# Optimization experiments

Measured on AMD Instinct MI355X. Metric: run time of the kernel, lower is better.

## Reference

```python
import jax, jax.numpy as jnp
import numpy as np

N_HEAD = 16
HEAD_DIM = 64
N_EMBD = N_HEAD * HEAD_DIM
KS, STRIDE = 4, 4
LN_EPS = 1e-5


def _layernorm(x, g, b):
    mu = jnp.mean(x, axis=-1, keepdims=True)
    var = jnp.var(x, axis=-1, keepdims=True)
    return (x - mu) * jax.lax.rsqrt(var + LN_EPS) * g + b


def _depthwise_conv(x_bcl, w):
    # x_bcl: [N, head_dim, L], w: [head_dim, 1, KS] (torch Conv1d groups=head_dim layout)
    return jax.lax.conv_general_dilated(
        x_bcl, w, window_strides=(STRIDE,), padding='VALID',
        dimension_numbers=('NCH', 'OIH', 'NCH'), feature_group_count=HEAD_DIM)


def setup_inputs() -> dict:
    key = jax.random.key(0)
    ks = jax.random.split(key, 12)
    B, T, L = 8, 64, 4096
    s = 0.02
    return {
        'x': jax.random.normal(ks[0], (B, T, N_EMBD), jnp.float32),
        'cached_k': jax.random.normal(ks[1], (B, N_HEAD, L, HEAD_DIM), jnp.float32),
        'cached_v': jax.random.normal(ks[2], (B, N_HEAD, L, HEAD_DIM), jnp.float32),
        'w_attn': jax.random.normal(ks[3], (N_EMBD, 3 * N_EMBD), jnp.float32) * s,
        'b_attn': jnp.zeros((3 * N_EMBD,), jnp.float32),
        'w_proj': jax.random.normal(ks[4], (N_EMBD, N_EMBD), jnp.float32) * s,
        'b_proj': jnp.zeros((N_EMBD,), jnp.float32),
        'k_conv': jax.random.normal(ks[5], (HEAD_DIM, 1, KS), jnp.float32) * 0.5,
        'v_conv': jax.random.normal(ks[6], (HEAD_DIM, 1, KS), jnp.float32) * 0.5,
        'ln_k_g': jnp.ones((HEAD_DIM,), jnp.float32),
        'ln_k_b': jnp.zeros((HEAD_DIM,), jnp.float32),
        'ln_v_g': jnp.ones((HEAD_DIM,), jnp.float32),
        'ln_v_b': jnp.zeros((HEAD_DIM,), jnp.float32),
    }


def reference(x, cached_k, cached_v, w_attn, b_attn, w_proj, b_proj,
              k_conv, v_conv, ln_k_g, ln_k_b, ln_v_g, ln_v_b):
    B, T, C = x.shape
    H, hd = N_HEAD, HEAD_DIM
    qkv = x @ w_attn + b_attn                      # [B,T,3C]
    q, k, v = jnp.split(qkv, 3, axis=-1)
    q = q.reshape(B, T, H, hd).transpose(0, 2, 1, 3)  # [B,H,T,hd]
    k = k.reshape(B, T, H, hd).transpose(0, 2, 1, 3)
    v = v.reshape(B, T, H, hd).transpose(0, 2, 1, 3)

    # compress cached K/V: depthwise conv over cache length, then LayerNorm
    L = cached_k.shape[2]
    pk = cached_k.transpose(0, 1, 3, 2).reshape(B * H, hd, L)
    pv = cached_v.transpose(0, 1, 3, 2).reshape(B * H, hd, L)
    ck = _depthwise_conv(pk, k_conv).reshape(B, H, hd, -1).transpose(0, 1, 3, 2)  # [B,H,Lc,hd]
    cv = _depthwise_conv(pv, v_conv).reshape(B, H, hd, -1).transpose(0, 1, 3, 2)
    ck = jax.lax.stop_gradient(_layernorm(ck, ln_k_g, ln_k_b))
    cv = jax.lax.stop_gradient(_layernorm(cv, ln_v_g, ln_v_b))

    k_full = jnp.concatenate([ck, k], axis=2)      # [B,H,Tk,hd]
    v_full = jnp.concatenate([cv, v], axis=2)
    Tk = k_full.shape[2]

    # faithful to original: rectangular tril(T, Tk) -> query i sees keys j<=i
    mask = jnp.tril(jnp.ones((T, Tk), dtype=bool))
    att = jnp.einsum('bhqd,bhkd->bhqk', q, k_full) * (1.0 / np.sqrt(hd))
    att = jnp.where(mask[None, None], att, -jnp.inf)
    att = jax.nn.softmax(att, axis=-1)
    y = jnp.einsum('bhqk,bhkd->bhqd', att, v_full)
    y = y.transpose(0, 2, 1, 3).reshape(B, T, C)
    return y @ w_proj + b_proj
```

## Files before the change

kernel.cpp:

```cpp
#include <hip/hip_runtime.h>
#include <math.h>

#define NH 16
#define LCACHE 4096

typedef __attribute__((ext_vector_type(8))) short short8;
typedef __attribute__((ext_vector_type(8))) unsigned short ushort8;
typedef __attribute__((ext_vector_type(4))) float f32x4;

__device__ __forceinline__ unsigned short f2bf(float f) {
    unsigned int u = __float_as_uint(f);
    u = (u + 0x7fffu + ((u >> 16) & 1u)) >> 16;
    return (unsigned short)u;
}

__global__ __launch_bounds__(256)
void pack_kernel(const float* __restrict__ x, const float* __restrict__ w_attn,
                 const float* __restrict__ w_proj,
                 ushort* __restrict__ xp, ushort* __restrict__ wq,
                 ushort* __restrict__ wp)
{
    __shared__ float Wt[64][65];
    const int bid = blockIdx.x, tid = threadIdx.x;
    const int w = tid >> 6, l = tid & 63;

    if (bid < 512) {
        const int isP = (bid >= 256);
        const int g2  = bid & 255;
        const int ntw = g2 >> 4, ktw = g2 & 15;
        const float* W = isP ? w_proj : w_attn;
        const int ldw  = isP ? 1024 : 3072;
        ushort* D      = isP ? wp : wq;
#pragma unroll
        for (int rep = 0; rep < 16; ++rep) {
            int lin = rep * 256 + tid;
            int kr = lin >> 6, nn = lin & 63;
            Wt[kr][nn] = W[(size_t)(ktw * 64 + kr) * ldw + ntw * 64 + nn];
        }
        __syncthreads();
        int r = l & 15, kg8 = l >> 4;
#pragma unroll
        for (int e = 0; e < 2; ++e) {
            int bi = w + e * 4;
            int kb = bi >> 2, nb = bi & 3;
            ushort8 o;
#pragma unroll
            for (int j = 0; j < 8; ++j)
                o[j] = f2bf(Wt[kb * 32 + kg8 * 8 + j][nb * 16 + r]);
            size_t f_lin = (size_t)(ntw * 16 + ktw) * 8 + bi;
            *(ushort8*)(D + f_lin * 512 + l * 8) = o;
        }
        return;
    }

    {
        int bid2 = bid - 512;
        int r = l & 15, kg8 = l >> 4;
#pragma unroll
        for (int i = 0; i < 4; ++i) {
            int f = bid2 * 16 + w * 4 + i;
            int mt = f >> 6, kt = (f >> 2) & 15, fi = f & 3;
            int kb = fi >> 1, mb = fi & 1;
            int m  = mt * 32 + mb * 16 + r;
            int k0 = kt * 64 + kb * 32 + kg8 * 8;
            const float* s = x + (size_t)m * 1024 + k0;
            ushort8 o;
#pragma unroll
            for (int j = 0; j < 8; ++j) o[j] = f2bf(s[j]);
            *(ushort8*)(xp + (size_t)f * 512 + l * 8) = o;
        }
    }
}

__global__ __launch_bounds__(512, 2)
void attn_kernel(const float* __restrict__ cached_k, const float* __restrict__ cached_v,
                 const float* __restrict__ kcw, const float* __restrict__ vcw,
                 const float* __restrict__ lkg, const float* __restrict__ lkb,
                 const float* __restrict__ lvg, const float* __restrict__ lvb,
                 const float* __restrict__ b_attn,
                 const ushort* __restrict__ xp, const ushort* __restrict__ wq,
                 ushort* __restrict__ yp)
{
    __shared__ __align__(16) float qs[32][68];
    __shared__ __align__(16) ushort P_lds[2048];
    __shared__ __align__(16) ushort ckf_s[4096];
    __shared__ __align__(16) ushort cvf_s[4096];

    const int bid = blockIdx.x;
    const int h    = ((bid & 7) << 1) | ((bid >> 3) & 1);
    const int rem  = bid >> 4;
    const int b    = rem >> 1;
    const int half = rem & 1;
    const int mtA  = b * 2 + half;

    const int tid = threadIdx.x;
    const int w = tid >> 6, l = tid & 63;
    const int c = l & 15, rg = l >> 4;
    const int g = w & 1, dup = w >> 1;

    {
        ushort8 z = {0,0,0,0,0,0,0,0};
        ((ushort8*)ckf_s)[tid] = z;
        ((ushort8*)cvf_s)[tid] = z;
    }
    __syncthreads();

    if (w >= 4) {
        const int cw = w - 4;
        const int NR = half ? 64 : 32;
        const float* Kb = cached_k + (size_t)(b * NH + h) * (LCACHE * 64);
        const float* Vb = cached_v + (size_t)(b * NH + h) * (LCACHE * 64);
        float4 wk = *(const float4*)(kcw + l * 4);
        float4 wv = *(const float4*)(vcw + l * 4);
        float gk = lkg[l], bk = lkb[l], gv = lvg[l], bv = lvb[l];

        const int iters = (2 * NR) / 4;
        for (int it = 0; it < iters; it += 4) {
            float tap[4][4]; int isKv[4], lcv[4];
#pragma unroll
            for (int q = 0; q < 4; ++q) {
                int t = cw + (it + q) * 4;
                isKv[q] = (t < NR);
                int lc = isKv[q] ? t : t - NR;
                lcv[q] = lc;
                const float* p = (isKv[q] ? Kb : Vb) + (size_t)lc * 256 + l;
                tap[q][0] = p[0]; tap[q][1] = p[64]; tap[q][2] = p[128]; tap[q][3] = p[192];
            }
            float av[4], s1[4], s2[4];
#pragma unroll
            for (int q = 0; q < 4; ++q) {
                float4 cwv = isKv[q] ? wk : wv;
                float a = tap[q][0] * cwv.x;
                a = fmaf(tap[q][1], cwv.y, a);
                a = fmaf(tap[q][2], cwv.z, a);
                a = fmaf(tap[q][3], cwv.w, a);
                av[q] = a; s1[q] = a; s2[q] = a * a;
            }
#pragma unroll
            for (int o = 32; o; o >>= 1) {
#pragma unroll
                for (int q = 0; q < 4; ++q) {
                    s1[q] += __shfl_xor(s1[q], o);
                    s2[q] += __shfl_xor(s2[q], o);
                }
            }
#pragma unroll
            for (int q = 0; q < 4; ++q) {
                float mu  = s1[q] * 0.015625f;
                float var = s2[q] * 0.015625f - mu * mu;
                float gg = isKv[q] ? gk : gv, bb2 = isKv[q] ? bk : bv;
                float outv = (av[q] - mu) * rsqrtf(var + 1e-5f) * gg + bb2;
                unsigned short bf = f2bf(outv);
                int key = lcv[q], d = l;
                if (isKv[q]) {
                    int off = ((key >> 4) * 2 + (d >> 5)) * 512
                            + ((d >> 3) & 3) * 128 + (key & 15) * 8 + (d & 7);
                    ckf_s[off] = bf;
                } else {
                    int off = ((d >> 4) * 2 + (key >> 5)) * 512
                            + ((key >> 3) & 3) * 128 + (d & 15) * 8 + (key & 7);
                    cvf_s[off] = bf;
                }
            }
        }
    } else {
        const ushort* ab = xp + (size_t)mtA * 32768;
        const ushort* bb = wq + (size_t)h * 65536;
        f32x4 acc0 = {0.f,0.f,0.f,0.f}, acc1 = {0.f,0.f,0.f,0.f};
#pragma unroll
        for (int kt = 0; kt < 16; ++kt) {
            const ushort* A = ab + kt * 2048;
            const ushort* B = bb + kt * 4096;
            short8 a00 = *(const short8*)(A + l * 8);
            short8 a01 = *(const short8*)(A + 512 + l * 8);
            short8 a10 = *(const short8*)(A + 1024 + l * 8);
            short8 a11 = *(const short8*)(A + 1536 + l * 8);
            short8 b0  = *(const short8*)(B + (size_t)w * 512 + l * 8);
            short8 b1  = *(const short8*)(B + (size_t)(4 + w) * 512 + l * 8);
            acc0 = __builtin_amdgcn_mfma_f32_16x16x32_bf16(a00, b0, acc0, 0, 0, 0);
            acc1 = __builtin_amdgcn_mfma_f32_16x16x32_bf16(a01, b0, acc1, 0, 0, 0);
            acc0 = __builtin_amdgcn_mfma_f32_16x16x32_bf16(a10, b1, acc0, 0, 0, 0);
            acc1 = __builtin_amdgcn_mfma_f32_16x16x32_bf16(a11, b1, acc1, 0, 0, 0);
        }
        const int n = w * 16 + c;
        float bv2 = b_attn[h * 64 + n];
#pragma unroll
        for (int mb = 0; mb < 2; ++mb) {
            f32x4 acc = mb ? acc1 : acc0;
#pragma unroll
            for (int rr = 0; rr < 4; ++rr)
                qs[mb * 16 + rg * 4 + rr][n] = (acc[rr] + bv2) * 0.125f;
        }
    }
    __syncthreads();

    short8 akf[4][2];
#pragma unroll
    for (int mf = 0; mf < 4; ++mf)
#pragma unroll
        for (int kf = 0; kf < 2; ++kf)
            akf[mf][kf] = *(const short8*)&ckf_s[(mf * 2 + kf) * 512 + l * 8];
    short8 avf[2];
#pragma unroll
    for (int kf = 0; kf < 2; ++kf)
        avf[kf] = *(const short8*)&cvf_s[(dup * 2 + kf) * 512 + l * 8];

    short8 qb[2];
#pragma unroll
    for (int kf = 0; kf < 2; ++kf) {
        int row = 16 * g + c;
        int d0  = 32 * kf + 8 * rg;
        float4 v0 = *(const float4*)&qs[row][d0];
        float4 v1 = *(const float4*)&qs[row][d0 + 4];
        ushort8 t;
        t[0] = f2bf(v0.x); t[1] = f2bf(v0.y); t[2] = f2bf(v0.z); t[3] = f2bf(v0.w);
        t[4] = f2bf(v1.x); t[5] = f2bf(v1.y); t[6] = f2bf(v1.z); t[7] = f2bf(v1.w);
        qb[kf] = (short8)t;
    }

    f32x4 sacc[4];
#pragma unroll
    for (int mf = 0; mf < 4; ++mf) { sacc[mf][0]=0.f; sacc[mf][1]=0.f; sacc[mf][2]=0.f; sacc[mf][3]=0.f; }
#pragma unroll
    for (int mf = 0; mf < 4; ++mf) {
        sacc[mf] = __builtin_amdgcn_mfma_f32_16x16x32_bf16(akf[mf][0], qb[0], sacc[mf], 0, 0, 0);
        sacc[mf] = __builtin_amdgcn_mfma_f32_16x16x32_bf16(akf[mf][1], qb[1], sacc[mf], 0, 0, 0);
    }

    const int gq = half * 32 + 16 * g + c;
    float pv[4][4];
    float mx = -3.0e38f;
#pragma unroll
    for (int mf = 0; mf < 4; ++mf)
#pragma unroll
        for (int rr = 0; rr < 4; ++rr) {
            int kidx = 16 * mf + 4 * rg + rr;
            float sc = (kidx <= gq) ? sacc[mf][rr] : -3.0e38f;
            pv[mf][rr] = sc;
            mx = fmaxf(mx, sc);
        }
    mx = fmaxf(mx, __shfl_xor(mx, 16));
    mx = fmaxf(mx, __shfl_xor(mx, 32));
    float sum = 0.f;
#pragma unroll
    for (int mf = 0; mf < 4; ++mf)
#pragma unroll
        for (int rr = 0; rr < 4; ++rr) {
            int kidx = 16 * mf + 4 * rg + rr;
            float e = (kidx <= gq) ? __expf(pv[mf][rr] - mx) : 0.f;
            pv[mf][rr] = e;
            sum += e;
        }
    sum += __shfl_xor(sum, 16);
    sum += __shfl_xor(sum, 32);
    float inv = 1.0f / sum;

    if (dup == 0) {
        int q = 16 * g + c;
        int swz = (q & 7) << 3;
#pragma unroll
        for (int mf = 0; mf < 4; ++mf)
#pragma unroll
            for (int rr = 0; rr < 4; ++rr) {
                int kidx = 16 * mf + 4 * rg + rr;
                P_lds[q * 64 + (kidx ^ swz)] = f2bf(pv[mf][rr] * inv);
            }
    }
    __syncthreads();

    short8 pb[2];
#pragma unroll
    for (int kf = 0; kf < 2; ++kf) {
        int q = 16 * g + c;
        int key0 = 32 * kf + 8 * rg;
        pb[kf] = *(const short8*)&P_lds[q * 64 + (key0 ^ ((q & 7) << 3))];
    }
    f32x4 oacc = {0.f, 0.f, 0.f, 0.f};
    oacc = __builtin_amdgcn_mfma_f32_16x16x32_bf16(avf[0], pb[0], oacc, 0, 0, 0);
    oacc = __builtin_amdgcn_mfma_f32_16x16x32_bf16(avf[1], pb[1], oacc, 0, 0, 0);

#pragma unroll
    for (int rr = 0; rr < 4; ++rr) {
        int d  = 16 * dup + 4 * rg + rr;
        int kb = d >> 5, ke = d & 31;
        int l2 = ((ke >> 3) << 4) | c;
        int j2 = ke & 7;
        size_t off = (size_t)mtA * 32768 + (size_t)h * 2048
                   + (size_t)(kb * 2 + g) * 512 + (size_t)l2 * 8 + j2;
        yp[off] = f2bf(oacc[rr]);
    }
}

__global__ __launch_bounds__(512, 2)
void gemm2_kernel(const ushort* __restrict__ Ap, const ushort* __restrict__ Bp,
                  const float* __restrict__ bias, float* __restrict__ C)
{
    __shared__ float red[32][68];

    const int bid = blockIdx.x;
    const int nt = ((bid & 7) << 1) | ((bid >> 3) & 1);
    const int mt = bid >> 4;
    const int tid = threadIdx.x;
    const int w = tid >> 6, l = tid & 63;
    const int kg = w >> 2, w4 = w & 3;
    const int c = l & 15, rg = l >> 4;

    const ushort* ab = Ap + (size_t)mt * 32768;
    const ushort* bb = Bp + (size_t)nt * 65536;
    f32x4 acc0 = {0.f,0.f,0.f,0.f}, acc1 = {0.f,0.f,0.f,0.f};
#pragma unroll
    for (int s = 0; s < 8; ++s) {
        const int kt = kg * 8 + s;
        const ushort* A = ab + kt * 2048;
        const ushort* B = bb + kt * 4096;
        short8 a00 = *(const short8*)(A + l * 8);
        short8 a01 = *(const short8*)(A + 512 + l * 8);
        short8 a10 = *(const short8*)(A + 1024 + l * 8);
        short8 a11 = *(const short8*)(A + 1536 + l * 8);
        short8 b0  = *(const short8*)(B + (size_t)w4 * 512 + l * 8);
        short8 b1  = *(const short8*)(B + (size_t)(4 + w4) * 512 + l * 8);
        acc0 = __builtin_amdgcn_mfma_f32_16x16x32_bf16(a00, b0, acc0, 0, 0, 0);
        acc1 = __builtin_amdgcn_mfma_f32_16x16x32_bf16(a01, b0, acc1, 0, 0, 0);
        acc0 = __builtin_amdgcn_mfma_f32_16x16x32_bf16(a10, b1, acc0, 0, 0, 0);
        acc1 = __builtin_amdgcn_mfma_f32_16x16x32_bf16(a11, b1, acc1, 0, 0, 0);
    }

    const int nl = w4 * 16 + c;
    if (kg == 0) {
#pragma unroll
        for (int mb = 0; mb < 2; ++mb) {
            f32x4 acc = mb ? acc1 : acc0;
#pragma unroll
            for (int rr = 0; rr < 4; ++rr)
                red[mb * 16 + rg * 4 + rr][nl] = acc[rr];
        }
    }
    __syncthreads();
    if (kg == 1) {
        float bv = bias[nt * 64 + nl];
#pragma unroll
        for (int mb = 0; mb < 2; ++mb) {
            f32x4 acc = mb ? acc1 : acc0;
#pragma unroll
            for (int rr = 0; rr < 4; ++rr) {
                int m = mb * 16 + rg * 4 + rr;
                C[(size_t)(mt * 32 + m) * 1024 + nt * 64 + nl] =
                    red[m][nl] + acc[rr] + bv;
            }
        }
    }
}

extern "C" void kernel_launch(void* const* d_in, const int* in_sizes, int n_in,
                              void* d_out, int out_size, void* d_ws, size_t ws_size,
                              hipStream_t stream)
{
    const float* x        = (const float*)d_in[0];
    const float* cached_k = (const float*)d_in[1];
    const float* cached_v = (const float*)d_in[2];
    const float* w_attn   = (const float*)d_in[3];
    const float* b_attn   = (const float*)d_in[4];
    const float* w_proj   = (const float*)d_in[5];
    const float* b_proj   = (const float*)d_in[6];
    const float* k_conv   = (const float*)d_in[7];
    const float* v_conv   = (const float*)d_in[8];
    const float* ln_k_g   = (const float*)d_in[9];
    const float* ln_k_b   = (const float*)d_in[10];
    const float* ln_v_g   = (const float*)d_in[11];
    const float* ln_v_b   = (const float*)d_in[12];

    ushort* xp = (ushort*)d_ws;
    ushort* wq = xp + 524288;
    ushort* wp = wq + 1048576;
    ushort* yp = wp + 1048576;
    float* out = (float*)d_out;

    pack_kernel<<<576, 256, 0, stream>>>(x, w_attn, w_proj, xp, wq, wp);
    attn_kernel<<<256, 512, 0, stream>>>(cached_k, cached_v, k_conv, v_conv,
                                         ln_k_g, ln_k_b, ln_v_g, ln_v_b,
                                         b_attn, xp, wq, yp);
    gemm2_kernel<<<256, 512, 0, stream>>>(yp, wp, b_proj, out);
}
```

Measured before the change: 30.09 us.

## Interleave cache conv/LN with Q GEMM across all waves; split proj GEMM finer

The attention kernel no longer splits waves into separate compress and GEMM roles. Every wave now issues its cached K/V tap loads up front, runs half of a split-K Q projection, does the conv+LayerNorm, then loads the second V batch and runs the other half, reducing the two K halves through LDS. This is meant to hide global load latency behind MFMA work and use all eight waves for both jobs. The projection GEMM moves to 512 blocks with a 4-way K split, XCD-aware tile mapping and a smaller reduction buffer, and f2bf switches to the library bf16 conversion. The risks are higher register pressure from the 64 held tap values (the occupancy hint of 2 was removed) and extra LDS synchronisation.

```diff
diff --git a/kernel.cpp b/kernel.cpp
--- a/kernel.cpp
+++ b/kernel.cpp
@@ -1,4 +1,5 @@
 #include <hip/hip_runtime.h>
+#include <hip/hip_bf16.h>
 #include <math.h>
 
 #define NH 16
@@ -9,9 +10,10 @@
 typedef __attribute__((ext_vector_type(4))) float f32x4;
 
 __device__ __forceinline__ unsigned short f2bf(float f) {
-    unsigned int u = __float_as_uint(f);
-    u = (u + 0x7fffu + ((u >> 16) & 1u)) >> 16;
-    return (unsigned short)u;
+    __hip_bfloat16 b = __float2bfloat16(f);
+    unsigned short u;
+    __builtin_memcpy(&u, &b, 2);
+    return u;
 }
 
 __global__ __launch_bounds__(256)
@@ -72,7 +74,7 @@
     }
 }
 
-__global__ __launch_bounds__(512, 2)
+__global__ __launch_bounds__(512)
 void attn_kernel(const float* __restrict__ cached_k, const float* __restrict__ cached_v,
                  const float* __restrict__ kcw, const float* __restrict__ vcw,
                  const float* __restrict__ lkg, const float* __restrict__ lkb,
@@ -83,8 +85,8 @@
 {
     __shared__ __align__(16) float qs[32][68];
     __shared__ __align__(16) ushort P_lds[2048];
-    __shared__ __align__(16) ushort ckf_s[4096];
-    __shared__ __align__(16) ushort cvf_s[4096];
+    __shared__ __align__(16) ushort ck_s[4096];
+    __shared__ __align__(16) ushort cv_s[4096];
 
     const int bid = blockIdx.x;
     const int h    = ((bid & 7) << 1) | ((bid >> 3) & 1);
@@ -95,221 +97,38 @@
 
     const int tid = threadIdx.x;
     const int w = tid >> 6, l = tid & 63;
+    const int kg = w >> 2, w4 = w & 3;
     const int c = l & 15, rg = l >> 4;
     const int g = w & 1, dup = w >> 1;
 
-    {
+    if (!half) {
         ushort8 z = {0,0,0,0,0,0,0,0};
-        ((ushort8*)ckf_s)[tid] = z;
-        ((ushort8*)cvf_s)[tid] = z;
+        ((ushort8*)cv_s)[tid] = z;
     }
     __syncthreads();
 
-    if (w >= 4) {
-        const int cw = w - 4;
-        const int NR = half ? 64 : 32;
-        const float* Kb = cached_k + (size_t)(b * NH + h) * (LCACHE * 64);
-        const float* Vb = cached_v + (size_t)(b * NH + h) * (LCACHE * 64);
-        float4 wk = *(const float4*)(kcw + l * 4);
-        float4 wv = *(const float4*)(vcw + l * 4);
-        float gk = lkg[l], bk = lkb[l], gv = lvg[l], bv = lvb[l];
-
-        const int iters = (2 * NR) / 4;
-        for (int it = 0; it < iters; it += 4) {
-            float tap[4][4]; int isKv[4], lcv[4];
-#pragma unroll
-            for (int q = 0; q < 4; ++q) {
-                int t = cw + (it + q) * 4;
-                isKv[q] = (t < NR);
-                int lc = isKv[q] ? t : t - NR;
-                lcv[q] = lc;
-                const float* p = (isKv[q] ? Kb : Vb) + (size_t)lc * 256 + l;
-                tap[q][0] = p[0]; tap[q][1] = p[64]; tap[q][2] = p[128]; tap[q][3] = p[192];
-            }
-            float av[4], s1[4], s2[4];
-#pragma unroll
-            for (int q = 0; q < 4; ++q) {
-                float4 cwv = isKv[q] ? wk : wv;
-                float a = tap[q][0] * cwv.x;
-                a = fmaf(tap[q][1], cwv.y, a);
-                a = fmaf(tap[q][2], cwv.z, a);
-                a = fmaf(tap[q][3], cwv.w, a);
-                av[q] = a; s1[q] = a; s2[q] = a * a;
-            }
-#pragma unroll
-            for (int o = 32; o; o >>= 1) {
-#pragma unroll
-                for (int q = 0; q < 4; ++q) {
-                    s1[q] += __shfl_xor(s1[q], o);
-                    s2[q] += __shfl_xor(s2[q], o);
-                }
-            }
-#pragma unroll
-            for (int q = 0; q < 4; ++q) {
-                float mu  = s1[q] * 0.015625f;
-                float var = s2[q] * 0.015625f - mu * mu;
-                float gg = isKv[q] ? gk : gv, bb2 = isKv[q] ? bk : bv;
-                float outv = (av[q] - mu) * rsqrtf(var + 1e-5f) * gg + bb2;
-                unsigned short bf = f2bf(outv);
-                int key = lcv[q], d = l;
-                if (isKv[q]) {
-                    int off = ((key >> 4) * 2 + (d >> 5)) * 512
-                            + ((d >> 3) & 3) * 128 + (key & 15) * 8 + (d & 7);
-                    ckf_s[off] = bf;
-                } else {
-                    int off = ((d >> 4) * 2 + (key >> 5)) * 512
-                            + ((key >> 3) & 3) * 128 + (d & 15) * 8 + (key & 7);
-                    cvf_s[off] = bf;
-                }
-            }
-        }
-    } else {
-        const ushort* ab = xp + (size_t)mtA * 32768;
-        const ushort* bb = wq + (size_t)h * 65536;
-        f32x4 acc0 = {0.f,0.f,0.f,0.f}, acc1 = {0.f,0.f,0.f,0.f};
-#pragma unroll
-        for (int kt = 0; kt < 16; ++kt) {
-            const ushort* A = ab + kt * 2048;
-            const ushort* B = bb + kt * 4096;
-            short8 a00 = *(const short8*)(A + l * 8);
-            short8 a01 = *(const short8*)(A + 512 + l * 8);
-            short8 a10 = *(const short8*)(A + 1024 + l * 8);
-            short8 a11 = *(const short8*)(A + 1536 + l * 8);
-            short8 b0  = *(const short8*)(B + (size_t)w * 512 + l * 8);
-            short8 b1  = *(const short8*)(B + (size_t)(4 + w) * 512 + l * 8);
-            acc0 = __builtin_amdgcn_mfma_f32_16x16x32_bf16(a00, b0, acc0, 0, 0, 0);
-            acc1 = __builtin_amdgcn_mfma_f32_16x16x32_bf16(a01, b0, acc1, 0, 0, 0);
-            acc0 = __builtin_amdgcn_mfma_f32_16x16x32_bf16(a10, b1, acc0, 0, 0, 0);
-            acc1 = __builtin_amdgcn_mfma_f32_16x16x32_bf16(a11, b1, acc1, 0, 0, 0);
-        }
-        const int n = w * 16 + c;
-        float bv2 = b_attn[h * 64 + n];
-#pragma unroll
-        for (int mb = 0; mb < 2; ++mb) {
-            f32x4 acc = mb ? acc1 : acc0;
-#pragma unroll
-            for (int rr = 0; rr < 4; ++rr)
-                qs[mb * 16 + rg * 4 + rr][n] = (acc[rr] + bv2) * 0.125f;
-        }
-    }
-    __syncthreads();
-
-    short8 akf[4][2];
-#pragma unroll
-    for (int mf = 0; mf < 4; ++mf)
-#pragma unroll
-        for (int kf = 0; kf < 2; ++kf)
-            akf[mf][kf] = *(const short8*)&ckf_s[(mf * 2 + kf) * 512 + l * 8];
-    short8 avf[2];
-#pragma unroll
-    for (int kf = 0; kf < 2; ++kf)
-        avf[kf] = *(const short8*)&cvf_s[(dup * 2 + kf) * 512 + l * 8];
-
-    short8 qb[2];
-#pragma unroll
-    for (int kf = 0; kf < 2; ++kf) {
-        int row = 16 * g + c;
-        int d0  = 32 * kf + 8 * rg;
-        float4 v0 = *(const float4*)&qs[row][d0];
-        float4 v1 = *(const float4*)&qs[row][d0 + 4];
-        ushort8 t;
-        t[0] = f2bf(v0.x); t[1] = f2bf(v0.y); t[2] = f2bf(v0.z); t[3] = f2bf(v0.w);
-        t[4] = f2bf(v1.x); t[5] = f2bf(v1.y); t[6] = f2bf(v1.z); t[7] = f2bf(v1.w);
-        qb[kf] = (short8)t;
-    }
-
-    f32x4 sacc[4];
-#pragma unroll
-    for (int mf = 0; mf < 4; ++mf) { sacc[mf][0]=0.f; sacc[mf][1]=0.f; sacc[mf][2]=0.f; sacc[mf][3]=0.f; }
-#pragma unroll
-    for (int mf = 0; mf < 4; ++mf) {
-        sacc[mf] = __builtin_amdgcn_mfma_f32_16x16x32_bf16(akf[mf][0], qb[0], sacc[mf], 0, 0, 0);
-        sacc[mf] = __builtin_amdgcn_mfma_f32_16x16x32_bf16(akf[mf][1], qb[1], sacc[mf], 0, 0, 0);
-    }
-
-    const int gq = half * 32 + 16 * g + c;
-    float pv[4][4];
-    float mx = -3.0e38f;
-#pragma unroll
-    for (int mf = 0; mf < 4; ++mf)
-#pragma unroll
-        for (int rr = 0; rr < 4; ++rr) {
-            int kidx = 16 * mf + 4 * rg + rr;
-            float sc = (kidx <= gq) ? sacc[mf][rr] : -3.0e38f;
-            pv[mf][rr] = sc;
-            mx = fmaxf(mx, sc);
-        }
-    mx = fmaxf(mx, __shfl_xor(mx, 16));
-    mx = fmaxf(mx, __shfl_xor(mx, 32));
-    float sum = 0.f;
-#pragma unroll
-    for (int mf = 0; mf < 4; ++mf)
-#pragma unroll
-        for (int rr = 0; rr < 4; ++rr) {
-            int kidx = 16 * mf + 4 * rg + rr;
-            float e = (kidx <= gq) ? __expf(pv[mf][rr] - mx) : 0.f;
-            pv[mf][rr] = e;
-            sum += e;
-        }
-    sum += __shfl_xor(sum, 16);
-    sum += __shfl_xor(sum, 32);
-    float inv = 1.0f / sum;
-
-    if (dup == 0) {
-        int q = 16 * g + c;
-        int swz = (q & 7) << 3;
-#pragma unroll
-        for (int mf = 0; mf < 4; ++mf)
-#pragma unroll
-            for (int rr = 0; rr < 4; ++rr) {
-                int kidx = 16 * mf + 4 * rg + rr;
-                P_lds[q * 64 + (kidx ^ swz)] = f2bf(pv[mf][rr] * inv);
-            }
-    }
-    __syncthreads();
-
-    short8 pb[2];
-#pragma unroll
-    for (int kf = 0; kf < 2; ++kf) {
-        int q = 16 * g + c;
-        int key0 = 32 * kf + 8 * rg;
-        pb[kf] = *(const short8*)&P_lds[q * 64 + (key0 ^ ((q & 7) << 3))];
-    }
-    f32x4 oacc = {0.f, 0.f, 0.f, 0.f};
-    oacc = __builtin_amdgcn_mfma_f32_16x16x32_bf16(avf[0], pb[0], oacc, 0, 0, 0);
-    oacc = __builtin_amdgcn_mfma_f32_16x16x32_bf16(avf[1], pb[1], oacc, 0, 0, 0);
-
-#pragma unroll
-    for (int rr = 0; rr < 4; ++rr) {
-        int d  = 16 * dup + 4 * rg + rr;
-        int kb = d >> 5, ke = d & 31;
-        int l2 = ((ke >> 3) << 4) | c;
-        int j2 = ke & 7;
-        size_t off = (size_t)mtA * 32768 + (size_t)h * 2048
-                   + (size_t)(kb * 2 + g) * 512 + (size_t)l2 * 8 + j2;
-        yp[off] = f2bf(oacc[rr]);
-    }
-}
-
-__global__ __launch_bounds__(512, 2)
-void gemm2_kernel(const ushort* __restrict__ Ap, const ushort* __restrict__ Bp,
-                  const float* __restrict__ bias, float* __restrict__ C)
-{
-    __shared__ float red[32][68];
-
-    const int bid = blockIdx.x;
-    const int nt = ((bid & 7) << 1) | ((bid >> 3) & 1);
-    const int mt = bid >> 4;
-    const int tid = threadIdx.x;
-    const int w = tid >> 6, l = tid & 63;
-    const int kg = w >> 2, w4 = w & 3;
-    const int c = l & 15, rg = l >> 4;
-
-    const ushort* ab = Ap + (size_t)mt * 32768;
-    const ushort* bb = Bp + (size_t)nt * 65536;
+    const float* Kb = cached_k + (size_t)(b * NH + h) * (LCACHE * 64);
+    const float* Vb = cached_v + (size_t)(b * NH + h) * (LCACHE * 64);
+    float tapA[8][4];
+#pragma unroll
+    for (int it = 0; it < 8; ++it) {
+        const float* src; int lc;
+        if (half) { lc = w + it * 8; src = Kb; }
+        else      { lc = w + (it & 3) * 8; src = (it < 4) ? Kb : Vb; }
+        const float* p = src + (size_t)lc * 256 + l;
+        tapA[it][0] = p[0]; tapA[it][1] = p[64];
+        tapA[it][2] = p[128]; tapA[it][3] = p[192];
+    }
+
+    float4 wk = *(const float4*)(kcw + l * 4);
+    float4 wv = *(const float4*)(vcw + l * 4);
+    float gk = lkg[l], bk = lkb[l], gv = lvg[l], bv = lvb[l];
+
+    const ushort* ab = xp + (size_t)mtA * 32768;
+    const ushort* bb = wq + (size_t)h * 65536;
     f32x4 acc0 = {0.f,0.f,0.f,0.f}, acc1 = {0.f,0.f,0.f,0.f};
 #pragma unroll
-    for (int s = 0; s < 8; ++s) {
+    for (int s = 0; s < 4; ++s) {
         const int kt = kg * 8 + s;
         const ushort* A = ab + kt * 2048;
         const ushort* B = bb + kt * 4096;
@@ -325,27 +144,289 @@
         acc1 = __builtin_amdgcn_mfma_f32_16x16x32_bf16(a11, b1, acc1, 0, 0, 0);
     }
 
-    const int nl = w4 * 16 + c;
-    if (kg == 0) {
+    {
+        float av[8], s1[8], s2[8];
+#pragma unroll
+        for (int it = 0; it < 8; ++it) {
+            bool isK = half ? true : (it < 4);
+            float4 cw = isK ? wk : wv;
+            float a = tapA[it][0] * cw.x;
+            a = fmaf(tapA[it][1], cw.y, a);
+            a = fmaf(tapA[it][2], cw.z, a);
+            a = fmaf(tapA[it][3], cw.w, a);
+            av[it] = a; s1[it] = a; s2[it] = a * a;
+        }
+#pragma unroll
+        for (int o = 32; o; o >>= 1) {
+#pragma unroll
+            for (int it = 0; it < 8; ++it) {
+                s1[it] += __shfl_xor(s1[it], o);
+                s2[it] += __shfl_xor(s2[it], o);
+            }
+        }
+#pragma unroll
+        for (int it = 0; it < 8; ++it) {
+            bool isK = half ? true : (it < 4);
+            int lc = half ? (w + it * 8) : (w + (it & 3) * 8);
+            float mu  = s1[it] * 0.015625f;
+            float var = s2[it] * 0.015625f - mu * mu;
+            float gg = isK ? gk : gv, bb2 = isK ? bk : bv;
+            unsigned short bf = f2bf((av[it] - mu) * rsqrtf(var + 1e-5f) * gg + bb2);
+            const int d = l, key = lc;
+            if (isK) {
+                int off = ((key >> 4) * 2 + (d >> 5)) * 512
+                        + ((d >> 3) & 3) * 128 + (key & 15) * 8 + (d & 7);
+                ck_s[off] = bf;
+            } else {
+                int off = ((d >> 4) * 2 + (key >> 5)) * 512
+                        + ((key >> 3) & 3) * 128 + (d & 15) * 8 + (key & 7);
+                cv_s[off] = bf;
+            }
+        }
+    }
+
+    float tapB[8][4];
+    if (half) {
+#pragma unroll
+        for (int it = 0; it < 8; ++it) {
+            int lc = w + it * 8;
+            const float* p = Vb + (size_t)lc * 256 + l;
+            tapB[it][0] = p[0]; tapB[it][1] = p[64];
+            tapB[it][2] = p[128]; tapB[it][3] = p[192];
+        }
+    }
+
+#pragma unroll
+    for (int s = 4; s < 8; ++s) {
+        const int kt = kg * 8 + s;
+        const ushort* A = ab + kt * 2048;
+        const ushort* B = bb + kt * 4096;
+        short8 a00 = *(const short8*)(A + l * 8);
+        short8 a01 = *(const short8*)(A + 512 + l * 8);
+        short8 a10 = *(const short8*)(A + 1024 + l * 8);
+        short8 a11 = *(const short8*)(A + 1536 + l * 8);
+        short8 b0  = *(const short8*)(B + (size_t)w4 * 512 + l * 8);
+        short8 b1  = *(const short8*)(B + (size_t)(4 + w4) * 512 + l * 8);
+        acc0 = __builtin_amdgcn_mfma_f32_16x16x32_bf16(a00, b0, acc0, 0, 0, 0);
+        acc1 = __builtin_amdgcn_mfma_f32_16x16x32_bf16(a01, b0, acc1, 0, 0, 0);
+        acc0 = __builtin_amdgcn_mfma_f32_16x16x32_bf16(a10, b1, acc0, 0, 0, 0);
+        acc1 = __builtin_amdgcn_mfma_f32_16x16x32_bf16(a11, b1, acc1, 0, 0, 0);
+    }
+
+    if (half) {
+        float av[8], s1[8], s2[8];
+#pragma unroll
+        for (int it = 0; it < 8; ++it) {
+            float a = tapB[it][0] * wv.x;
+            a = fmaf(tapB[it][1], wv.y, a);
+            a = fmaf(tapB[it][2], wv.z, a);
+            a = fmaf(tapB[it][3], wv.w, a);
+            av[it] = a; s1[it] = a; s2[it] = a * a;
+        }
+#pragma unroll
+        for (int o = 32; o; o >>= 1) {
+#pragma unroll
+            for (int it = 0; it < 8; ++it) {
+                s1[it] += __shfl_xor(s1[it], o);
+                s2[it] += __shfl_xor(s2[it], o);
+            }
+        }
+#pragma unroll
+        for (int it = 0; it < 8; ++it) {
+            int key = w + it * 8;
+            float mu  = s1[it] * 0.015625f;
+            float var = s2[it] * 0.015625f - mu * mu;
+            unsigned short bf = f2bf((av[it] - mu) * rsqrtf(var + 1e-5f) * gv + bv);
+            const int d = l;
+            int off = ((d >> 4) * 2 + (key >> 5)) * 512
+                    + ((key >> 3) & 3) * 128 + (d & 15) * 8 + (key & 7);
+            cv_s[off] = bf;
+        }
+    }
+
+    {
+        const int n = w4 * 16 + c;
+        if (kg == 0) {
+#pragma unroll
+            for (int mb = 0; mb < 2; ++mb) {
+                f32x4 acc = mb ? acc1 : acc0;
+#pragma unroll
+                for (int rr = 0; rr < 4; ++rr)
+                    qs[mb * 16 + rg * 4 + rr][n] = acc[rr];
+            }
+        }
+        __syncthreads();
+        if (kg == 1) {
+            float bv2 = b_attn[h * 64 + n];
+#pragma unroll
+            for (int mb = 0; mb < 2; ++mb) {
+                f32x4 acc = mb ? acc1 : acc0;
+#pragma unroll
+                for (int rr = 0; rr < 4; ++rr) {
+                    int m = mb * 16 + rg * 4 + rr;
+                    qs[m][n] = (qs[m][n] + acc[rr] + bv2) * 0.125f;
+                }
+            }
+        }
+        __syncthreads();
+    }
+
+    short8 akf[4][2];
+#pragma unroll
+    for (int mf = 0; mf < 4; ++mf)
+#pragma unroll
+        for (int kf = 0; kf < 2; ++kf)
+            akf[mf][kf] = *(const short8*)&ck_s[(mf * 2 + kf) * 512 + l * 8];
+    short8 avf[2];
+#pragma unroll
+    for (int kf = 0; kf < 2; ++kf)
+        avf[kf] = *(const short8*)&cv_s[(dup * 2 + kf) * 512 + l * 8];
+
+    short8 qb[2];
+#pragma unroll
+    for (int kf = 0; kf < 2; ++kf) {
+        int row = 16 * g + c;
+        int d0  = 32 * kf + 8 * rg;
+        float4 v0 = *(const float4*)&qs[row][d0];
+        float4 v1 = *(const float4*)&qs[row][d0 + 4];
+        ushort8 t;
+        t[0] = f2bf(v0.x); t[1] = f2bf(v0.y); t[2] = f2bf(v0.z); t[3] = f2bf(v0.w);
+        t[4] = f2bf(v1.x); t[5] = f2bf(v1.y); t[6] = f2bf(v1.z); t[7] = f2bf(v1.w);
+        qb[kf] = (short8)t;
+    }
+
+    f32x4 sacc[4];
+#pragma unroll
+    for (int mf = 0; mf < 4; ++mf) { sacc[mf][0]=0.f; sacc[mf][1]=0.f; sacc[mf][2]=0.f; sacc[mf][3]=0.f; }
+#pragma unroll
+    for (int mf = 0; mf < 4; ++mf) {
+        sacc[mf] = __builtin_amdgcn_mfma_f32_16x16x32_bf16(akf[mf][0], qb[0], sacc[mf], 0, 0, 0);
+        sacc[mf] = __builtin_amdgcn_mfma_f32_16x16x32_bf16(akf[mf][1], qb[1], sacc[mf], 0, 0, 0);
+    }
+
+    const int gq = half * 32 + 16 * g + c;
+    float pv[4][4];
+    float mx = -3.0e38f;
+#pragma unroll
+    for (int mf = 0; mf < 4; ++mf)
+#pragma unroll
+        for (int rr = 0; rr < 4; ++rr) {
+            int kidx = 16 * mf + 4 * rg + rr;
+            float sc = (kidx <= gq) ? sacc[mf][rr] : -3.0e38f;
+            pv[mf][rr] = sc;
+            mx = fmaxf(mx, sc);
+        }
+    mx = fmaxf(mx, __shfl_xor(mx, 16));
+    mx = fmaxf(mx, __shfl_xor(mx, 32));
+    float sum = 0.f;
+#pragma unroll
+    for (int mf = 0; mf < 4; ++mf)
+#pragma unroll
+        for (int rr = 0; rr < 4; ++rr) {
+            int kidx = 16 * mf + 4 * rg + rr;
+            float e = (kidx <= gq) ? __expf(pv[mf][rr] - mx) : 0.f;
+            pv[mf][rr] = e;
+            sum += e;
+        }
+    sum += __shfl_xor(sum, 16);
+    sum += __shfl_xor(sum, 32);
+    float inv = 1.0f / sum;
+
+    if (dup == 0) {
+        int q = 16 * g + c;
+        int swz = (q & 7) << 3;
+#pragma unroll
+        for (int mf = 0; mf < 4; ++mf)
+#pragma unroll
+            for (int rr = 0; rr < 4; ++rr) {
+                int kidx = 16 * mf + 4 * rg + rr;
+                P_lds[q * 64 + (kidx ^ swz)] = f2bf(pv[mf][rr] * inv);
+            }
+    }
+    __syncthreads();
+
+    short8 pb[2];
+#pragma unroll
+    for (int kf = 0; kf < 2; ++kf) {
+        int q = 16 * g + c;
+        int key0 = 32 * kf + 8 * rg;
+        pb[kf] = *(const short8*)&P_lds[q * 64 + (key0 ^ ((q & 7) << 3))];
+    }
+    f32x4 oacc = {0.f, 0.f, 0.f, 0.f};
+    oacc = __builtin_amdgcn_mfma_f32_16x16x32_bf16(avf[0], pb[0], oacc, 0, 0, 0);
+    oacc = __builtin_amdgcn_mfma_f32_16x16x32_bf16(avf[1], pb[1], oacc, 0, 0, 0);
+
+#pragma unroll
+    for (int rr = 0; rr < 4; ++rr) {
+        int d  = 16 * dup + 4 * rg + rr;
+        int kb = d >> 5, ke = d & 31;
+        int l2 = ((ke >> 3) << 4) | c;
+        int j2 = ke & 7;
+        size_t off = (size_t)mtA * 32768 + (size_t)h * 2048
+                   + (size_t)(kb * 2 + g) * 512 + (size_t)l2 * 8 + j2;
+        yp[off] = f2bf(oacc[rr]);
+    }
+}
+
+__global__ __launch_bounds__(512, 2)
+void gemm2_kernel(const ushort* __restrict__ Ap, const ushort* __restrict__ Bp,
+                  const float* __restrict__ bias, float* __restrict__ C)
+{
+    __shared__ float red[3][2][32][18];
+
+    const int bid = blockIdx.x;
+    const int xcd = bid & 7, idx = bid >> 3;
+    const int nt2 = xcd * 4 + (idx & 3);
+    const int mt  = idx >> 2;
+    const int nt  = nt2 >> 1;
+    const int tid = threadIdx.x;
+    const int w = tid >> 6, l = tid & 63;
+    const int kg = w >> 1, nb2 = w & 1;
+    const int nb = (nt2 & 1) * 2 + nb2;
+    const int c = l & 15, rg = l >> 4;
+
+    const ushort* ab = Ap + (size_t)mt * 32768;
+    const ushort* bb = Bp + (size_t)nt * 65536;
+    f32x4 acc0 = {0.f,0.f,0.f,0.f}, acc1 = {0.f,0.f,0.f,0.f};
+#pragma unroll
+    for (int s = 0; s < 4; ++s) {
+        const int kt = kg * 4 + s;
+        const ushort* A = ab + kt * 2048;
+        const ushort* B = bb + kt * 4096;
+        short8 a00 = *(const short8*)(A + l * 8);
+        short8 a01 = *(const short8*)(A + 512 + l * 8);
+        short8 a10 = *(const short8*)(A + 1024 + l * 8);
+        short8 a11 = *(const short8*)(A + 1536 + l * 8);
+        short8 b0  = *(const short8*)(B + (size_t)nb * 512 + l * 8);
+        short8 b1  = *(const short8*)(B + (size_t)(4 + nb) * 512 + l * 8);
+        acc0 = __builtin_amdgcn_mfma_f32_16x16x32_bf16(a00, b0, acc0, 0, 0, 0);
+        acc1 = __builtin_amdgcn_mfma_f32_16x16x32_bf16(a01, b0, acc1, 0, 0, 0);
+        acc0 = __builtin_amdgcn_mfma_f32_16x16x32_bf16(a10, b1, acc0, 0, 0, 0);
+        acc1 = __builtin_amdgcn_mfma_f32_16x16x32_bf16(a11, b1, acc1, 0, 0, 0);
+    }
+
+    if (kg > 0) {
 #pragma unroll
         for (int mb = 0; mb < 2; ++mb) {
             f32x4 acc = mb ? acc1 : acc0;
 #pragma unroll
             for (int rr = 0; rr < 4; ++rr)
-                red[mb * 16 + rg * 4 + rr][nl] = acc[rr];
+                red[kg - 1][nb2][mb * 16 + rg * 4 + rr][c] = acc[rr];
         }
     }
     __syncthreads();
-    if (kg == 1) {
-        float bv = bias[nt * 64 + nl];
+    if (kg == 0) {
+        const int n = nt2 * 32 + nb2 * 16 + c;
+        float bv = bias[n];
 #pragma unroll
         for (int mb = 0; mb < 2; ++mb) {
             f32x4 acc = mb ? acc1 : acc0;
 #pragma unroll
             for (int rr = 0; rr < 4; ++rr) {
                 int m = mb * 16 + rg * 4 + rr;
-                C[(size_t)(mt * 32 + m) * 1024 + nt * 64 + nl] =
-                    red[m][nl] + acc[rr] + bv;
+                float v = acc[rr] + red[0][nb2][m][c] + red[1][nb2][m][c]
+                        + red[2][nb2][m][c] + bv;
+                C[(size_t)(mt * 32 + m) * 1024 + n] = v;
             }
         }
     }
@@ -379,5 +460,5 @@
     attn_kernel<<<256, 512, 0, stream>>>(cached_k, cached_v, k_conv, v_conv,
                                          ln_k_g, ln_k_b, ln_v_g, ln_v_b,
                                          b_attn, xp, wq, yp);
-    gemm2_kernel<<<256, 512, 0, stream>>>(yp, wp, b_proj, out);
+    gemm2_kernel<<<512, 512, 0, stream>>>(yp, wp, b_proj, out);
 }
```

Result: faster. 27.84 us (-7.5%).
